# Kernel optimization log

Hardware: AMD Instinct MI355X
Metric: run time of the kernel (lower is better)

The kernel has to match this reference:

```python
import jax, jax.numpy as jnp
import numpy as np

# ---- config (mirrors AAModel init kwargs: ns=48, nv=10, sh_lmax=1) ----
N, E, NS, NV = 100000, 60000, 48, 10
SED, DED = 32, 32          # sigma / distance embedding dims
CUTOFF = 30.0              # GaussianSmearing(0, cutoff, DED)
SQ3 = float(np.sqrt(3.0))
W1_NUMEL = NS * NS + NS * NV                                   # 2784
# layer-2 fully-connected TP path weight offsets:
#   0e(x)0e->0e, 0e(x)1o->1o, 1o(x)0e->1o, 1o(x)1o->0e, 1o(x)1o->1e
O2 = [2304, 2784, 2884, 3364, 3464]


def _mlp2(x, W1, b1, W2, b2):
    return jax.nn.relu(x @ W1 + b1) @ W2 + b2


def _seg_mean(x, idx, n):
    s = jax.ops.segment_sum(x, idx, num_segments=n)
    cnt = jax.ops.segment_sum(jnp.ones(idx.shape, x.dtype), idx, num_segments=n)
    return s / jnp.maximum(cnt, 1.0).reshape((n,) + (1,) * (x.ndim - 1))


def _forward(pos, node_sigma_emb, node_s, edge_W1, edge_b1, edge_W2, edge_b2,
             fc1_W1, fc1_b1, fc1_W2, fc1_b2, fc2_W1, fc2_b1, fc2_W2, fc2_b2,
             edge_index):
    src, dst = edge_index[0], edge_index[1]
    vec = pos[dst] - pos[src]                          # [E,3]
    d = jnp.linalg.norm(vec, axis=-1)                  # [E]
    sh1 = SQ3 * vec / (d[:, None] + 1e-8)              # l=1 SH, component norm; sh0 == 1
    # Gaussian smearing of edge distances
    offsets = jnp.linspace(0.0, CUTOFF, DED)
    coeff = -0.5 / (offsets[1] - offsets[0]) ** 2
    demb = jnp.exp(coeff * (d[:, None] - offsets) ** 2)          # [E,DED]
    edge_emb = _mlp2(jnp.concatenate([node_sigma_emb[src], demb], -1),
                     edge_W1, edge_b1, edge_W2, edge_b2)         # [E,NS]

    # ---- conv layer 1:  ns x0e  (x)  1x0e+1x1o  ->  ns x0e + nv x1o ----
    xs = node_s[src]
    ea = jnp.concatenate([edge_emb, node_s[src], node_s[dst]], -1)   # [E,3*NS]
    w = _mlp2(ea, fc1_W1, fc1_b1, fc1_W2, fc1_b2)                    # [E,2784]
    w00 = w[:, :NS * NS].reshape(-1, NS, NS)
    w01 = w[:, NS * NS:].reshape(-1, NS, NV)
    inv = 1.0 / np.sqrt(NS)
    m_s = jnp.einsum('eio,ei->eo', w00, xs) * inv                    # [E,NS]
    m_v = jnp.einsum('eio,ei->eo', w01, xs)[:, :, None] * sh1[:, None, :] * inv  # [E,NV,3]
    node_s1 = node_s + _seg_mean(m_s, dst, N)                        # residual
    node_v1 = _seg_mean(m_v, dst, N)

    # ---- conv layer 2:  ns x0e + nv x1o  (x)  1x0e+1x1o  ->  ns x0e + nv x1o + nv x1e ----
    ea2 = jnp.concatenate([edge_emb, node_s1[src], node_s1[dst]], -1)
    w2 = _mlp2(ea2, fc2_W1, fc2_b1, fc2_W2, fc2_b2)                  # [E,3464]
    w00 = w2[:, :O2[0]].reshape(-1, NS, NS)
    w01 = w2[:, O2[0]:O2[1]].reshape(-1, NS, NV)
    w10 = w2[:, O2[1]:O2[2]].reshape(-1, NV, NV)
    w11s = w2[:, O2[2]:O2[3]].reshape(-1, NV, NS)
    w11p = w2[:, O2[3]:O2[4]].reshape(-1, NV, NV)
    xs, xv = node_s1[src], node_v1[src]
    nA = 1.0 / np.sqrt(2 * NS)
    nB = 1.0 / np.sqrt(2 * NV)
    m_s = (jnp.einsum('eio,ei->eo', w00, xs) * nA
           + jnp.einsum('eio,eid,ed->eo', w11s, xv, sh1) * (nB / SQ3))
    m_v = (jnp.einsum('eio,ei->eo', w01, xs)[:, :, None] * sh1[:, None, :] * nA
           + jnp.einsum('eio,eid->eod', w10, xv) * nB)
    m_p = jnp.einsum('eio,eid->eod', w11p, jnp.cross(xv, sh1[:, None, :])) * (1.0 / np.sqrt(2.0 * NV))
    node_s2 = node_s1 + _seg_mean(m_s, dst, N)
    node_v2 = node_v1 + _seg_mean(m_v, dst, N)
    node_p = _seg_mean(m_p, dst, N)
    # final node irreps ns x0e + nv x1o + nv x1e, flattened -> [N, 108]
    return jnp.concatenate([node_s2, node_v2.reshape(N, -1), node_p.reshape(N, -1)], -1)


def setup_inputs() -> dict:
    key = jax.random.key(0)
    k = jax.random.split(key, 10)
    f32 = jnp.float32
    def lin(kk, fi, fo):
        return jax.random.normal(kk, (fi, fo), f32) / np.sqrt(fi)
    return {
        'pos': 10.0 * jax.random.normal(k[0], (N, 3), f32),
        'node_sigma_emb': jax.random.normal(k[1], (N, SED), f32),
        'node_s': jax.random.normal(k[2], (N, NS), f32),
        'edge_W1': lin(k[3], SED + DED, NS), 'edge_b1': jnp.zeros((NS,), f32),
        'edge_W2': lin(k[4], NS, NS), 'edge_b2': jnp.zeros((NS,), f32),
        'fc1_W1': lin(k[5], 3 * NS, 3 * NS), 'fc1_b1': jnp.zeros((3 * NS,), f32),
        'fc1_W2': lin(k[6], 3 * NS, W1_NUMEL), 'fc1_b2': jnp.zeros((W1_NUMEL,), f32),
        'fc2_W1': lin(k[7], 3 * NS, 3 * NS), 'fc2_b1': jnp.zeros((3 * NS,), f32),
        'fc2_W2': lin(k[8], 3 * NS, O2[-1]), 'fc2_b2': jnp.zeros((O2[-1],), f32),
        'edge_index': jax.random.randint(k[9], (2, E), 0, N, jnp.int32),
    }


def reference(pos, node_sigma_emb, node_s, edge_W1, edge_b1, edge_W2, edge_b2,
              fc1_W1, fc1_b1, fc1_W2, fc1_b2, fc2_W1, fc2_b1, fc2_W2, fc2_b2,
              edge_index):
    return _forward(pos, node_sigma_emb, node_s, edge_W1, edge_b1, edge_W2, edge_b2,
                    fc1_W1, fc1_b1, fc1_W2, fc1_b2, fc2_W1, fc2_b1, fc2_W2, fc2_b2,
                    edge_index)
```

## Files before the change

### kernel.cpp

```cpp
#include <hip/hip_runtime.h>
#include <math.h>


constexpr float SQ3f = 1.7320508075688772f;
constexpr float INV1 = 0.14433756729740643f;
constexpr float NAc  = 0.10206207261596575f;
constexpr float NBc  = 0.22360679774997896f;
constexpr float NB3  = 0.12909944487358055f;
constexpr float C20  = 0.22360679774997896f;
constexpr float RATIO= 1.2649110640673518f;
constexpr float DSP  = 30.0f/31.0f;
constexpr float GCOEF= -0.5f/(DSP*DSP);

typedef __attribute__((ext_vector_type(8))) short bf16x8;
typedef __attribute__((ext_vector_type(4))) float f32x4;

__device__ __forceinline__ unsigned short f2bf(float x) {
    unsigned u = __builtin_bit_cast(unsigned, x);
    u += 0x7fffu + ((u >> 16) & 1u);
    return (unsigned short)(u >> 16);
}

__device__ __forceinline__ int colmap(int layer, int t, int lm) {
    if (layer == 0) return t*16 + lm;
    if (layer == 1) {
        if (t < 144) { const int og=t/48, i=t-og*48; return i*48 + og*16 + lm; }
        const int i = t-144; return (lm<10) ? 2304 + i*10 + lm : -1;
    }
    if (t < 144) { const int og=t/48, i=t-og*48; return i*48 + og*16 + lm; }
    if (t < 174) { const int s=t-144, og=s/10, i=s-og*10; return 2884 + i*48 + og*16 + lm; }
    if (t < 222) { const int i=t-174; return (lm<10) ? 2304 + i*10 + lm : -1; }
    if (t < 232) { const int i=t-222; return (lm<10) ? 2784 + i*10 + lm : -1; }
    { const int i=t-232; return (lm<10) ? 3364 + i*10 + lm : -1; }
}

__global__ __launch_bounds__(256)
void cvt_swz(const float* __restrict__ W, const float* __restrict__ bias,
             short* __restrict__ Wsw, int ncol, int ntile, int layer)
{
    const int gid = blockIdx.x*256 + threadIdx.x;
    const int g = gid >> 6, lane = gid & 63;
    if (g >= ntile*5) return;
    const int tile = g/5, ks = g - tile*5;
    const int c  = colmap(layer, tile, lane & 15);
    const int k0 = ks*32 + (lane >> 4)*8;
    union { uint4 u4; unsigned short h[8]; } pk;
    #pragma unroll
    for (int j=0;j<8;j++) {
        const int k = k0 + j;
        float v = 0.f;
        if (c >= 0) {
            if (k < 144)       v = W[(size_t)k*ncol + c];
            else if (k == 144) v = bias[c];
        }
        pk.h[j] = f2bf(v);
    }
    *(uint4*)&Wsw[((size_t)g*64 + lane)*8] = pk.u4;
}

__global__ __launch_bounds__(256)
void edge_kernel(const float* __restrict__ pos, const float* __restrict__ sigma,
                 const int* __restrict__ ei,
                 const float* __restrict__ W1, const float* __restrict__ b1,
                 const float* __restrict__ W2, const float* __restrict__ b2,
                 float* __restrict__ edge_emb, float* __restrict__ sh1buf,
                 int* __restrict__ deg, int E)
{
    __shared__ float inl[4][64];
    __shared__ float hidl[4][48];
    const int w    = threadIdx.x >> 6;
    const int lane = threadIdx.x & 63;
    const int e    = blockIdx.x*4 + w;
    const bool valid = (e < E);
    const int ec = valid ? e : 0;
    const int src = ei[ec], dst = ei[E+ec];
    const float vx = pos[dst*3+0]-pos[src*3+0];
    const float vy = pos[dst*3+1]-pos[src*3+1];
    const float vz = pos[dst*3+2]-pos[src*3+2];
    const float d  = sqrtf(vx*vx+vy*vy+vz*vz);
    const float si = SQ3f/(d+1e-8f);
    const float s0 = vx*si, s1 = vy*si, s2 = vz*si;
    if (lane < 32) {
        inl[w][lane] = sigma[src*32+lane];
    } else {
        const float off  = (float)(lane-32)*DSP;
        const float diff = d - off;
        inl[w][lane] = expf(GCOEF*diff*diff);
    }
    __syncthreads();
    if (lane < 48) {
        float a = b1[lane];
        #pragma unroll 8
        for (int j=0;j<64;j++) a = fmaf(inl[w][j], W1[j*48+lane], a);
        hidl[w][lane] = fmaxf(a, 0.f);
    }
    __syncthreads();
    if (valid) {
        if (lane < 48) {
            float a = b2[lane];
            #pragma unroll 8
            for (int j=0;j<48;j++) a = fmaf(hidl[w][j], W2[j*48+lane], a);
            edge_emb[e*48+lane] = a;
        }
        if (lane == 0) atomicAdd(&deg[dst], 1);
        if (lane < 3)  sh1buf[e*4+lane] = (lane==0)?s0:((lane==1)?s1:s2);
    }
}

__device__ __forceinline__ void load_bfrag(const short* __restrict__ Wsw,
                                           int tile, int lane, bf16x8 (&b)[5]) {
    #pragma unroll
    for (int ks=0; ks<5; ks++)
        b[ks] = *(const bf16x8*)&Wsw[((size_t)(tile*5+ks)*64 + lane)*8];
}

template<typename F>
__device__ __forceinline__ void region(const short* __restrict__ Wsw, int base,
                                       int count, int wv, int lane,
                                       const bf16x8 (&ag)[2][5], F&& upd)
{
    bf16x8 bc[5], bn[5];
    int i = wv;
    if (i < count) load_bfrag(Wsw, base+i, lane, bc);
    for (; i < count; i += 4) {
        if (i+4 < count) load_bfrag(Wsw, base+i+4, lane, bn);
        f32x4 a0 = {0.f,0.f,0.f,0.f}, a1 = {0.f,0.f,0.f,0.f};
        #pragma unroll
        for (int ks=0; ks<5; ks++) {
            a0 = __builtin_amdgcn_mfma_f32_16x16x32_bf16(ag[0][ks], bc[ks], a0, 0,0,0);
            a1 = __builtin_amdgcn_mfma_f32_16x16x32_bf16(ag[1][ks], bc[ks], a1, 0,0,0);
        }
        upd(i, a0, a1);
        #pragma unroll
        for (int ks=0; ks<5; ks++) bc[ks] = bn[ks];
    }
}

template<int LAYER>
__global__ __launch_bounds__(256, 2)
void conv_kernel(const float* __restrict__ edge_emb, const float* __restrict__ sh1buf,
                 const int* __restrict__ ei,
                 const float* __restrict__ sin_, const float* __restrict__ vin,
                 const short* __restrict__ W1sw, const short* __restrict__ W2sw,
                 float* __restrict__ outS, float* __restrict__ outV, int E)
{
    constexpr int POOL_FL = (LAYER==1) ? 7552 : 8960;
    __shared__ __align__(16) float pool[POOL_FL];
    __shared__ __align__(16) short hidB[32*192];
    __shared__ float xsL[32*49];
    __shared__ float sh1l[32][4];
    __shared__ int   srcl[32], dstl[32];
    __shared__ float xvL[LAYER==2 ? 32*30 : 1];
    __shared__ float uL [LAYER==2 ? 32*10 : 1];
    __shared__ float cvL[LAYER==2 ? 32*30 : 1];

    short* eaB = (short*)pool;

    const int t  = threadIdx.x;
    const int eb = blockIdx.x * 32;

    if (t < 32) {
        const int ge = eb + t; const int gc = (ge < E) ? ge : (E-1);
        srcl[t] = ei[gc]; dstl[t] = ei[E+gc];
    }
    if (t < 128) {
        const int e = t >> 2, k = t & 3;
        const int ge = eb + e; const int gc = (ge<E)?ge:(E-1);
        sh1l[e][k] = sh1buf[gc*4 + k];
    }
    __syncthreads();

    for (int p = t; p < 32*24; p += 256) {
        const int m = p / 24, s = p - m*24;
        const int k0 = s*8;
        float vals[8] = {0.f,0.f,0.f,0.f,0.f,0.f,0.f,0.f};
        if (k0 < 48) {
            const int ge = eb + m; const int gc = (ge<E)?ge:(E-1);
            const float4 a = *(const float4*)&edge_emb[gc*48 + k0];
            const float4 b = *(const float4*)&edge_emb[gc*48 + k0 + 4];
            vals[0]=a.x; vals[1]=a.y; vals[2]=a.z; vals[3]=a.w;
            vals[4]=b.x; vals[5]=b.y; vals[6]=b.z; vals[7]=b.w;
        } else if (k0 < 96) {
            const float4 a = *(const float4*)&sin_[srcl[m]*48 + (k0-48)];
            const float4 b = *(const float4*)&sin_[srcl[m]*48 + (k0-48) + 4];
            vals[0]=a.x; vals[1]=a.y; vals[2]=a.z; vals[3]=a.w;
            vals[4]=b.x; vals[5]=b.y; vals[6]=b.z; vals[7]=b.w;
            #pragma unroll
            for (int j=0;j<8;j++) xsL[m*49 + (k0-48) + j] = vals[j];
        } else if (k0 < 144) {
            const float4 a = *(const float4*)&sin_[dstl[m]*48 + (k0-96)];
            const float4 b = *(const float4*)&sin_[dstl[m]*48 + (k0-96) + 4];
            vals[0]=a.x; vals[1]=a.y; vals[2]=a.z; vals[3]=a.w;
            vals[4]=b.x; vals[5]=b.y; vals[6]=b.z; vals[7]=b.w;
        } else if (k0 == 144) {
            vals[0] = 1.f;
        }
        union { uint4 u4; unsigned short h[8]; } pk;
        #pragma unroll
        for (int j=0;j<8;j++) pk.h[j] = f2bf(vals[j]);
        *(uint4*)&eaB[m*192 + ((s ^ (m&7))*8)] = pk.u4;
    }
    if (t < 64) {
        const int m = t >> 1, s = 18 + (t & 1);
        union { uint4 u4; unsigned short h[8]; } pk;
        pk.u4.x = pk.u4.y = pk.u4.z = pk.u4.w = 0u;
        if (s == 18) pk.h[0] = f2bf(1.f);
        *(uint4*)&hidB[m*192 + ((s ^ (m&7))*8)] = pk.u4;
    }
    if (LAYER==2) {
        for (int p=t; p<320; p+=256) {
            const int e = p/10, i = p - e*10;
            const float* vp = &vin[srcl[e]*30 + i*3];
            const float x0=vp[0], x1=vp[1], x2=vp[2];
            const float h0=sh1l[e][0], h1=sh1l[e][1], h2=sh1l[e][2];
            xvL[e*30+i*3+0]=x0; xvL[e*30+i*3+1]=x1; xvL[e*30+i*3+2]=x2;
            uL[e*10+i] = x0*h0 + x1*h1 + x2*h2;
            cvL[e*30+i*3+0] = x1*h2 - x2*h1;
            cvL[e*30+i*3+1] = x2*h0 - x0*h2;
            cvL[e*30+i*3+2] = x0*h1 - x1*h0;
        }
    }
    __syncthreads();

    const int wv = t >> 6, lane = t & 63;
    const int lm = lane & 15, lk = lane >> 4;
    const int lk4 = lk*4;

    {
        bf16x8 af[2][5];
        #pragma unroll
        for (int mt=0; mt<2; mt++) {
            const int m = mt*16 + lm;
            #pragma unroll
            for (int ks=0; ks<5; ks++)
                af[mt][ks] = *(const bf16x8*)&eaB[m*192 + (((ks*4+lk) ^ (m&7))*8)];
        }
        for (int nt = wv; nt < 9; nt += 4) {
            bf16x8 bf_[5];
            load_bfrag(W1sw, nt, lane, bf_);
            f32x4 a0 = {0.f,0.f,0.f,0.f}, a1 = {0.f,0.f,0.f,0.f};
            #pragma unroll
            for (int ks=0; ks<5; ks++) {
                a0 = __builtin_amdgcn_mfma_f32_16x16x32_bf16(af[0][ks], bf_[ks], a0, 0,0,0);
                a1 = __builtin_amdgcn_mfma_f32_16x16x32_bf16(af[1][ks], bf_[ks], a1, 0,0,0);
            }
            const int c = nt*16 + lm;
            #pragma unroll
            for (int r=0; r<4; r++) {
                const int m0 = lk4 + r, m1 = 16 + lk4 + r;
                hidB[m0*192 + (((c>>3) ^ (m0&7))*8) + (c&7)] = (short)f2bf(fmaxf(a0[r], 0.f));
                hidB[m1*192 + (((c>>3) ^ (m1&7))*8) + (c&7)] = (short)f2bf(fmaxf(a1[r], 0.f));
            }
        }
    }
    __syncthreads();

    bf16x8 ag[2][5];
    #pragma unroll
    for (int mt=0; mt<2; mt++) {
        const int m = mt*16 + lm;
        #pragma unroll
        for (int ks=0; ks<5; ks++)
            ag[mt][ks] = *(const bf16x8*)&hidB[m*192 + (((ks*4+lk) ^ (m&7))*8)];
    }

    for (int og=0; og<3; og++) {
        float ms[2][4] = {{0.f,0.f,0.f,0.f},{0.f,0.f,0.f,0.f}};
        region(W2sw, og*48, 48, wv, lane, ag, [&](int i, f32x4 a0, f32x4 a1) {
            #pragma unroll
            for (int r=0; r<4; r++) {
                ms[0][r] = fmaf(a0[r], xsL[(lk4+r)*49 + i],      ms[0][r]);
                ms[1][r] = fmaf(a1[r], xsL[(16+lk4+r)*49 + i],   ms[1][r]);
            }
        });
        if (LAYER==2) {
            region(W2sw, 144+og*10, 10, wv, lane, ag, [&](int i, f32x4 a0, f32x4 a1) {
                #pragma unroll
                for (int r=0; r<4; r++) {
                    ms[0][r] = fmaf(a0[r]*RATIO, uL[(lk4+r)*10 + i],    ms[0][r]);
                    ms[1][r] = fmaf(a1[r]*RATIO, uL[(16+lk4+r)*10 + i], ms[1][r]);
                }
            });
        }
        #pragma unroll
        for (int r=0; r<4; r++) {
            pool[wv*1568 + (lk4+r)*49    + og*16+lm] = ms[0][r];
            pool[wv*1568 + (16+lk4+r)*49 + og*16+lm] = ms[1][r];
        }
    }

    if (LAYER==1) {
        float mv[2][4] = {{0.f,0.f,0.f,0.f},{0.f,0.f,0.f,0.f}};
        region(W2sw, 144, 48, wv, lane, ag, [&](int i, f32x4 a0, f32x4 a1) {
            #pragma unroll
            for (int r=0; r<4; r++) {
                mv[0][r] = fmaf(a0[r], xsL[(lk4+r)*49 + i],    mv[0][r]);
                mv[1][r] = fmaf(a1[r], xsL[(16+lk4+r)*49 + i], mv[1][r]);
            }
        });
        if (lm < 10) {
            #pragma unroll
            for (int r=0; r<4; r++) {
                pool[6272 + wv*320 + (lk4+r)*10    + lm] = mv[0][r];
                pool[6272 + wv*320 + (16+lk4+r)*10 + lm] = mv[1][r];
            }
        }
        __syncthreads();
        for (int p=t; p<1536; p+=256) {
            const int e = p/48, o = p - (p/48)*48;
            if (eb+e < E) {
                const int a = e*49 + o;
                const float v = pool[a] + pool[1568+a] + pool[3136+a] + pool[4704+a];
                unsafeAtomicAdd(&outS[dstl[e]*48 + o], v*INV1);
            }
        }
        for (int p=t; p<320; p+=256) {
            const int e = p/10, o = p - (p/10)*10;
            if (eb+e < E) {
                const int a = 6272 + e*10 + o;
                float v = pool[a] + pool[a+320] + pool[a+640] + pool[a+960];
                v *= INV1;
                #pragma unroll
                for (int d=0; d<3; d++)
                    unsafeAtomicAdd(&outV[dstl[e]*30 + o*3 + d], v*sh1l[e][d]);
            }
        }
    } else {
        __syncthreads();
        for (int p=t; p<1536; p+=256) {
            const int e = p/48, o = p - (p/48)*48;
            if (eb+e < E) {
                const int a = e*49 + o;
                const float v = pool[a] + pool[1568+a] + pool[3136+a] + pool[4704+a];
                unsafeAtomicAdd(&outS[dstl[e]*108 + o], v*NAc);
            }
        }
        __syncthreads();

        {
            float mv[2][4] = {{0.f,0.f,0.f,0.f},{0.f,0.f,0.f,0.f}};
            region(W2sw, 174, 48, wv, lane, ag, [&](int i, f32x4 a0, f32x4 a1) {
                #pragma unroll
                for (int r=0; r<4; r++) {
                    mv[0][r] = fmaf(a0[r], xsL[(lk4+r)*49 + i],    mv[0][r]);
                    mv[1][r] = fmaf(a1[r], xsL[(16+lk4+r)*49 + i], mv[1][r]);
                }
            });
            if (lm < 10) {
                #pragma unroll
                for (int r=0; r<4; r++) {
                    pool[wv*320 + (lk4+r)*10    + lm] = mv[0][r];
                    pool[wv*320 + (16+lk4+r)*10 + lm] = mv[1][r];
                }
            }
        }
        {
            float m3[2][4][3] = {};
            region(W2sw, 222, 10, wv, lane, ag, [&](int i, f32x4 a0, f32x4 a1) {
                #pragma unroll
                for (int r=0; r<4; r++)
                    #pragma unroll
                    for (int d=0; d<3; d++) {
                        m3[0][r][d] = fmaf(a0[r], xvL[(lk4+r)*30 + i*3 + d],    m3[0][r][d]);
                        m3[1][r][d] = fmaf(a1[r], xvL[(16+lk4+r)*30 + i*3 + d], m3[1][r][d]);
                    }
            });
            if (lm < 10) {
                #pragma unroll
                for (int r=0; r<4; r++)
                    #pragma unroll
                    for (int d=0; d<3; d++) {
                        pool[1280 + wv*960 + (lk4+r)*30    + lm*3 + d] = m3[0][r][d];
                        pool[1280 + wv*960 + (16+lk4+r)*30 + lm*3 + d] = m3[1][r][d];
                    }
            }
        }
        {
            float m3[2][4][3] = {};
            region(W2sw, 232, 10, wv, lane, ag, [&](int i, f32x4 a0, f32x4 a1) {
                #pragma unroll
                for (int r=0; r<4; r++)
                    #pragma unroll
                    for (int d=0; d<3; d++) {
                        m3[0][r][d] = fmaf(a0[r], cvL[(lk4+r)*30 + i*3 + d],    m3[0][r][d]);
                        m3[1][r][d] = fmaf(a1[r], cvL[(16+lk4+r)*30 + i*3 + d], m3[1][r][d]);
                    }
            });
            if (lm < 10) {
                #pragma unroll
                for (int r=0; r<4; r++)
                    #pragma unroll
                    for (int d=0; d<3; d++) {
                        pool[5120 + wv*960 + (lk4+r)*30    + lm*3 + d] = m3[0][r][d];
                        pool[5120 + wv*960 + (16+lk4+r)*30 + lm*3 + d] = m3[1][r][d];
                    }
            }
        }
        __syncthreads();
        for (int p=t; p<320; p+=256) {
            const int e = p/10, o = p - (p/10)*10;
            if (eb+e < E) {
                const int a = e*10 + o;
                const float vc = pool[a] + pool[a+320] + pool[a+640] + pool[a+960];
                const int base = dstl[e]*108;
                #pragma unroll
                for (int d=0; d<3; d++) {
                    const int b = e*30 + o*3 + d;
                    const float vv = pool[1280+b] + pool[1280+960+b] + pool[1280+1920+b] + pool[1280+2880+b];
                    const float pp = pool[5120+b] + pool[5120+960+b] + pool[5120+1920+b] + pool[5120+2880+b];
                    unsafeAtomicAdd(&outS[base + 48 + o*3 + d], vc*NAc*sh1l[e][d] + vv*NBc);
                    unsafeAtomicAdd(&outS[base + 78 + o*3 + d], pp*C20);
                }
            }
        }
    }
}

__global__ __launch_bounds__(256)
void fin1_kernel(const float* __restrict__ node_s, const int* __restrict__ deg,
                 float* __restrict__ s1, float* __restrict__ v1, int Nn)
{
    const int p = blockIdx.x*256 + threadIdx.x;
    const int totS = Nn*48;
    if (p < totS) {
        const int n = p/48;
        const int dgi = deg[n];
        const float dg = (float)(dgi > 1 ? dgi : 1);
        s1[p] = node_s[p] + s1[p]/dg;
    } else {
        const int q = p - totS;
        if (q < Nn*30) {
            const int n = q/30;
            const int dgi = deg[n];
            const float dg = (float)(dgi > 1 ? dgi : 1);
            v1[q] = v1[q]/dg;
        }
    }
}

__global__ __launch_bounds__(256)
void fin2_kernel(const float* __restrict__ s1, const float* __restrict__ v1,
                 const int* __restrict__ deg, float* __restrict__ out, int Nn)
{
    const int p = blockIdx.x*256 + threadIdx.x;
    if (p >= Nn*108) return;
    const int n = p/108, c = p - n*108;
    const int dgi = deg[n];
    const float dg = (float)(dgi > 1 ? dgi : 1);
    const float acc = out[p]/dg;
    if (c < 48)      out[p] = s1[n*48+c] + acc;
    else if (c < 78) out[p] = v1[n*30 + (c-48)] + acc;
    else             out[p] = acc;
}

extern "C" void kernel_launch(void* const* d_in, const int* in_sizes, int n_in,
                              void* d_out, int out_size, void* d_ws, size_t ws_size,
                              hipStream_t stream)
{
    const float* pos    = (const float*)d_in[0];
    const float* sigma  = (const float*)d_in[1];
    const float* node_s = (const float*)d_in[2];
    const float* eW1  = (const float*)d_in[3];
    const float* eb1  = (const float*)d_in[4];
    const float* eW2  = (const float*)d_in[5];
    const float* eb2  = (const float*)d_in[6];
    const float* f1W1 = (const float*)d_in[7];
    const float* f1b1 = (const float*)d_in[8];
    const float* f1W2 = (const float*)d_in[9];
    const float* f1b2 = (const float*)d_in[10];
    const float* f2W1 = (const float*)d_in[11];
    const float* f2b1 = (const float*)d_in[12];
    const float* f2W2 = (const float*)d_in[13];
    const float* f2b2 = (const float*)d_in[14];
    const int*   ei   = (const int*)d_in[15];
    const int Nn = in_sizes[0]/3;
    const int E  = in_sizes[15]/2;
    float* out = (float*)d_out;

    char* ws = (char*)d_ws;
    float* edge_emb = (float*)ws;  ws += (size_t)E*48*sizeof(float);
    float* sh1buf   = (float*)ws;  ws += (size_t)E*4*sizeof(float);
    float* s1       = (float*)ws;  ws += (size_t)Nn*48*sizeof(float);
    float* v1       = (float*)ws;  ws += (size_t)Nn*30*sizeof(float);
    int*   deg      = (int*)ws;    ws += (size_t)Nn*sizeof(int);
    short* W1sw     = (short*)ws;  ws += (size_t)9*5*64*8*sizeof(short);
    short* W2sw     = (short*)ws;  ws += (size_t)242*5*64*8*sizeof(short);

    hipMemsetAsync(s1,  0, (size_t)Nn*48*sizeof(float), stream);
    hipMemsetAsync(v1,  0, (size_t)Nn*30*sizeof(float), stream);
    hipMemsetAsync(deg, 0, (size_t)Nn*sizeof(int),      stream);
    hipMemsetAsync(out, 0, (size_t)Nn*108*sizeof(float), stream);

    edge_kernel<<<(E+3)/4, 256, 0, stream>>>(pos, sigma, ei, eW1, eb1, eW2, eb2,
                                             edge_emb, sh1buf, deg, E);

    cvt_swz<<<(9*5*64+255)/256,   256, 0, stream>>>(f1W1, f1b1, W1sw, 144, 9, 0);
    cvt_swz<<<(192*5*64+255)/256, 256, 0, stream>>>(f1W2, f1b2, W2sw, 2784, 192, 1);

    conv_kernel<1><<<(E+31)/32, 256, 0, stream>>>(edge_emb, sh1buf, ei, node_s, nullptr,
                                                  W1sw, W2sw, s1, v1, E);
    fin1_kernel<<<((size_t)Nn*78 + 255)/256, 256, 0, stream>>>(node_s, deg, s1, v1, Nn);

    cvt_swz<<<(9*5*64+255)/256,   256, 0, stream>>>(f2W1, f2b1, W1sw, 144, 9, 0);
    cvt_swz<<<(242*5*64+255)/256, 256, 0, stream>>>(f2W2, f2b2, W2sw, 3464, 242, 2);

    conv_kernel<2><<<(E+31)/32, 256, 0, stream>>>(edge_emb, sh1buf, ei, s1, v1,
                                                  W1sw, W2sw, out, nullptr, E);
    fin2_kernel<<<((size_t)Nn*108 + 255)/256, 256, 0, stream>>>(s1, v1, deg, out, Nn);
}
```

Baseline: 428.6 us.

## Assign output groups to waves and atomically scatter directly from MFMA registers

Instead of each of the four waves taking a strided share of every weight tile and then reducing partial sums through a large shared-memory pool, each wave now owns whole output groups. Waves 0-2 each handle one 16-column scalar slice and wave 3 handles the vector paths, and each wave issues global atomics straight from its accumulators. Per-edge scalar and vector inputs are stored transposed in LDS so they can be read as float4 vectors, and the weight fragments are double-buffered explicitly. Dropping the pool frees LDS and removes barriers, so the occupancy hint rises from 2 to 4 blocks per CU, at the cost of uneven work across waves in layer 2.

```diff
diff --git a/kernel.cpp b/kernel.cpp
--- a/kernel.cpp
+++ b/kernel.cpp
@@ -6,7 +6,6 @@
 constexpr float INV1 = 0.14433756729740643f;
 constexpr float NAc  = 0.10206207261596575f;
 constexpr float NBc  = 0.22360679774997896f;
-constexpr float NB3  = 0.12909944487358055f;
 constexpr float C20  = 0.22360679774997896f;
 constexpr float RATIO= 1.2649110640673518f;
 constexpr float DSP  = 30.0f/31.0f;
@@ -114,47 +113,33 @@
         b[ks] = *(const bf16x8*)&Wsw[((size_t)(tile*5+ks)*64 + lane)*8];
 }
 
-template<typename F>
-__device__ __forceinline__ void region(const short* __restrict__ Wsw, int base,
-                                       int count, int wv, int lane,
-                                       const bf16x8 (&ag)[2][5], F&& upd)
-{
-    bf16x8 bc[5], bn[5];
-    int i = wv;
-    if (i < count) load_bfrag(Wsw, base+i, lane, bc);
-    for (; i < count; i += 4) {
-        if (i+4 < count) load_bfrag(Wsw, base+i+4, lane, bn);
-        f32x4 a0 = {0.f,0.f,0.f,0.f}, a1 = {0.f,0.f,0.f,0.f};
-        #pragma unroll
-        for (int ks=0; ks<5; ks++) {
-            a0 = __builtin_amdgcn_mfma_f32_16x16x32_bf16(ag[0][ks], bc[ks], a0, 0,0,0);
-            a1 = __builtin_amdgcn_mfma_f32_16x16x32_bf16(ag[1][ks], bc[ks], a1, 0,0,0);
-        }
-        upd(i, a0, a1);
-        #pragma unroll
-        for (int ks=0; ks<5; ks++) bc[ks] = bn[ks];
+__device__ __forceinline__ void mfma5(const bf16x8 (&ag)[2][5], const bf16x8 (&b)[5],
+                                      f32x4& a0, f32x4& a1) {
+    a0 = (f32x4){0.f,0.f,0.f,0.f};
+    a1 = (f32x4){0.f,0.f,0.f,0.f};
+    #pragma unroll
+    for (int ks=0; ks<5; ks++) {
+        a0 = __builtin_amdgcn_mfma_f32_16x16x32_bf16(ag[0][ks], b[ks], a0, 0,0,0);
+        a1 = __builtin_amdgcn_mfma_f32_16x16x32_bf16(ag[1][ks], b[ks], a1, 0,0,0);
     }
 }
 
 template<int LAYER>
-__global__ __launch_bounds__(256, 2)
+__global__ __launch_bounds__(256, 4)
 void conv_kernel(const float* __restrict__ edge_emb, const float* __restrict__ sh1buf,
                  const int* __restrict__ ei,
                  const float* __restrict__ sin_, const float* __restrict__ vin,
                  const short* __restrict__ W1sw, const short* __restrict__ W2sw,
                  float* __restrict__ outS, float* __restrict__ outV, int E)
 {
-    constexpr int POOL_FL = (LAYER==1) ? 7552 : 8960;
-    __shared__ __align__(16) float pool[POOL_FL];
+    __shared__ __align__(16) short eaB[32*192];
     __shared__ __align__(16) short hidB[32*192];
-    __shared__ float xsL[32*49];
+    __shared__ __align__(16) float xsT[48][32];
     __shared__ float sh1l[32][4];
     __shared__ int   srcl[32], dstl[32];
-    __shared__ float xvL[LAYER==2 ? 32*30 : 1];
-    __shared__ float uL [LAYER==2 ? 32*10 : 1];
-    __shared__ float cvL[LAYER==2 ? 32*30 : 1];
-
-    short* eaB = (short*)pool;
+    __shared__ __align__(16) float xvT[LAYER==2 ? 30 : 1][32];
+    __shared__ __align__(16) float uT [LAYER==2 ? 10 : 1][32];
+    __shared__ __align__(16) float cvT[LAYER==2 ? 30 : 1][32];
 
     const int t  = threadIdx.x;
     const int eb = blockIdx.x * 32;
@@ -185,8 +170,6 @@
             const float4 b = *(const float4*)&sin_[srcl[m]*48 + (k0-48) + 4];
             vals[0]=a.x; vals[1]=a.y; vals[2]=a.z; vals[3]=a.w;
             vals[4]=b.x; vals[5]=b.y; vals[6]=b.z; vals[7]=b.w;
-            #pragma unroll
-            for (int j=0;j<8;j++) xsL[m*49 + (k0-48) + j] = vals[j];
         } else if (k0 < 144) {
             const float4 a = *(const float4*)&sin_[dstl[m]*48 + (k0-96)];
             const float4 b = *(const float4*)&sin_[dstl[m]*48 + (k0-96) + 4];
@@ -207,24 +190,28 @@
         if (s == 18) pk.h[0] = f2bf(1.f);
         *(uint4*)&hidB[m*192 + ((s ^ (m&7))*8)] = pk.u4;
     }
+    for (int p=t; p<1536; p+=256) {
+        const int k = p >> 5, e = p & 31;
+        xsT[k][e] = sin_[srcl[e]*48 + k];
+    }
     if (LAYER==2) {
         for (int p=t; p<320; p+=256) {
-            const int e = p/10, i = p - e*10;
-            const float* vp = &vin[srcl[e]*30 + i*3];
-            const float x0=vp[0], x1=vp[1], x2=vp[2];
+            const int i = p >> 5, e = p & 31;
+            const float x0 = vin[srcl[e]*30 + i*3+0];
+            const float x1 = vin[srcl[e]*30 + i*3+1];
+            const float x2 = vin[srcl[e]*30 + i*3+2];
             const float h0=sh1l[e][0], h1=sh1l[e][1], h2=sh1l[e][2];
-            xvL[e*30+i*3+0]=x0; xvL[e*30+i*3+1]=x1; xvL[e*30+i*3+2]=x2;
-            uL[e*10+i] = x0*h0 + x1*h1 + x2*h2;
-            cvL[e*30+i*3+0] = x1*h2 - x2*h1;
-            cvL[e*30+i*3+1] = x2*h0 - x0*h2;
-            cvL[e*30+i*3+2] = x0*h1 - x1*h0;
+            xvT[i*3+0][e]=x0; xvT[i*3+1][e]=x1; xvT[i*3+2][e]=x2;
+            uT[i][e] = x0*h0 + x1*h1 + x2*h2;
+            cvT[i*3+0][e] = x1*h2 - x2*h1;
+            cvT[i*3+1][e] = x2*h0 - x0*h2;
+            cvT[i*3+2][e] = x0*h1 - x1*h0;
         }
     }
     __syncthreads();
 
     const int wv = t >> 6, lane = t & 63;
-    const int lm = lane & 15, lk = lane >> 4;
-    const int lk4 = lk*4;
+    const int lm = lane & 15, lk = lane >> 4, lk4 = lk*4;
 
     {
         bf16x8 af[2][5];
@@ -236,14 +223,10 @@
                 af[mt][ks] = *(const bf16x8*)&eaB[m*192 + (((ks*4+lk) ^ (m&7))*8)];
         }
         for (int nt = wv; nt < 9; nt += 4) {
-            bf16x8 bf_[5];
-            load_bfrag(W1sw, nt, lane, bf_);
-            f32x4 a0 = {0.f,0.f,0.f,0.f}, a1 = {0.f,0.f,0.f,0.f};
-            #pragma unroll
-            for (int ks=0; ks<5; ks++) {
-                a0 = __builtin_amdgcn_mfma_f32_16x16x32_bf16(af[0][ks], bf_[ks], a0, 0,0,0);
-                a1 = __builtin_amdgcn_mfma_f32_16x16x32_bf16(af[1][ks], bf_[ks], a1, 0,0,0);
-            }
+            bf16x8 bw[5];
+            load_bfrag(W1sw, nt, lane, bw);
+            f32x4 a0, a1;
+            mfma5(af, bw, a0, a1);
             const int c = nt*16 + lm;
             #pragma unroll
             for (int r=0; r<4; r++) {
@@ -264,152 +247,219 @@
             ag[mt][ks] = *(const bf16x8*)&hidB[m*192 + (((ks*4+lk) ^ (m&7))*8)];
     }
 
-    for (int og=0; og<3; og++) {
+    if (wv < 3) {
         float ms[2][4] = {{0.f,0.f,0.f,0.f},{0.f,0.f,0.f,0.f}};
-        region(W2sw, og*48, 48, wv, lane, ag, [&](int i, f32x4 a0, f32x4 a1) {
-            #pragma unroll
-            for (int r=0; r<4; r++) {
-                ms[0][r] = fmaf(a0[r], xsL[(lk4+r)*49 + i],      ms[0][r]);
-                ms[1][r] = fmaf(a1[r], xsL[(16+lk4+r)*49 + i],   ms[1][r]);
-            }
-        });
+        {
+            bf16x8 b0[5], b1_[5];
+            const int base = wv*48;
+            load_bfrag(W2sw, base, lane, b0);
+            for (int i=0; i<48; i+=2) {
+                load_bfrag(W2sw, base+i+1, lane, b1_);
+                f32x4 a0, a1;
+                mfma5(ag, b0, a0, a1);
+                {
+                    const f32x4 x0 = *(const f32x4*)&xsT[i][lk4];
+                    const f32x4 x1 = *(const f32x4*)&xsT[i][16+lk4];
+                    #pragma unroll
+                    for (int r=0;r<4;r++) {
+                        ms[0][r] = fmaf(a0[r], x0[r], ms[0][r]);
+                        ms[1][r] = fmaf(a1[r], x1[r], ms[1][r]);
+                    }
+                }
+                if (i+2 < 48) load_bfrag(W2sw, base+i+2, lane, b0);
+                mfma5(ag, b1_, a0, a1);
+                {
+                    const f32x4 x0 = *(const f32x4*)&xsT[i+1][lk4];
+                    const f32x4 x1 = *(const f32x4*)&xsT[i+1][16+lk4];
+                    #pragma unroll
+                    for (int r=0;r<4;r++) {
+                        ms[0][r] = fmaf(a0[r], x0[r], ms[0][r]);
+                        ms[1][r] = fmaf(a1[r], x1[r], ms[1][r]);
+                    }
+                }
+            }
+        }
         if (LAYER==2) {
-            region(W2sw, 144+og*10, 10, wv, lane, ag, [&](int i, f32x4 a0, f32x4 a1) {
-                #pragma unroll
-                for (int r=0; r<4; r++) {
-                    ms[0][r] = fmaf(a0[r]*RATIO, uL[(lk4+r)*10 + i],    ms[0][r]);
-                    ms[1][r] = fmaf(a1[r]*RATIO, uL[(16+lk4+r)*10 + i], ms[1][r]);
-                }
-            });
-        }
+            bf16x8 b0[5], b1_[5];
+            const int base = 144 + wv*10;
+            load_bfrag(W2sw, base, lane, b0);
+            for (int i=0; i<10; i+=2) {
+                load_bfrag(W2sw, base+i+1, lane, b1_);
+                f32x4 a0, a1;
+                mfma5(ag, b0, a0, a1);
+                {
+                    const f32x4 u0 = *(const f32x4*)&uT[i][lk4];
+                    const f32x4 u1 = *(const f32x4*)&uT[i][16+lk4];
+                    #pragma unroll
+                    for (int r=0;r<4;r++) {
+                        ms[0][r] = fmaf(a0[r]*RATIO, u0[r], ms[0][r]);
+                        ms[1][r] = fmaf(a1[r]*RATIO, u1[r], ms[1][r]);
+                    }
+                }
+                if (i+2 < 10) load_bfrag(W2sw, base+i+2, lane, b0);
+                mfma5(ag, b1_, a0, a1);
+                {
+                    const f32x4 u0 = *(const f32x4*)&uT[i+1][lk4];
+                    const f32x4 u1 = *(const f32x4*)&uT[i+1][16+lk4];
+                    #pragma unroll
+                    for (int r=0;r<4;r++) {
+                        ms[0][r] = fmaf(a0[r]*RATIO, u0[r], ms[0][r]);
+                        ms[1][r] = fmaf(a1[r]*RATIO, u1[r], ms[1][r]);
+                    }
+                }
+            }
+        }
+        const float scale = (LAYER==1) ? INV1 : NAc;
+        const int   strd  = (LAYER==1) ? 48 : 108;
+        const int o = wv*16 + lm;
         #pragma unroll
-        for (int r=0; r<4; r++) {
-            pool[wv*1568 + (lk4+r)*49    + og*16+lm] = ms[0][r];
-            pool[wv*1568 + (16+lk4+r)*49 + og*16+lm] = ms[1][r];
-        }
-    }
-
-    if (LAYER==1) {
-        float mv[2][4] = {{0.f,0.f,0.f,0.f},{0.f,0.f,0.f,0.f}};
-        region(W2sw, 144, 48, wv, lane, ag, [&](int i, f32x4 a0, f32x4 a1) {
-            #pragma unroll
-            for (int r=0; r<4; r++) {
-                mv[0][r] = fmaf(a0[r], xsL[(lk4+r)*49 + i],    mv[0][r]);
-                mv[1][r] = fmaf(a1[r], xsL[(16+lk4+r)*49 + i], mv[1][r]);
-            }
-        });
-        if (lm < 10) {
-            #pragma unroll
-            for (int r=0; r<4; r++) {
-                pool[6272 + wv*320 + (lk4+r)*10    + lm] = mv[0][r];
-                pool[6272 + wv*320 + (16+lk4+r)*10 + lm] = mv[1][r];
-            }
-        }
-        __syncthreads();
-        for (int p=t; p<1536; p+=256) {
-            const int e = p/48, o = p - (p/48)*48;
-            if (eb+e < E) {
-                const int a = e*49 + o;
-                const float v = pool[a] + pool[1568+a] + pool[3136+a] + pool[4704+a];
-                unsafeAtomicAdd(&outS[dstl[e]*48 + o], v*INV1);
-            }
-        }
-        for (int p=t; p<320; p+=256) {
-            const int e = p/10, o = p - (p/10)*10;
-            if (eb+e < E) {
-                const int a = 6272 + e*10 + o;
-                float v = pool[a] + pool[a+320] + pool[a+640] + pool[a+960];
-                v *= INV1;
-                #pragma unroll
-                for (int d=0; d<3; d++)
-                    unsafeAtomicAdd(&outV[dstl[e]*30 + o*3 + d], v*sh1l[e][d]);
-            }
+        for (int r=0;r<4;r++) {
+            const int e0 = lk4+r, e1 = 16+lk4+r;
+            if (eb+e0 < E) unsafeAtomicAdd(&outS[(size_t)dstl[e0]*strd + o], ms[0][r]*scale);
+            if (eb+e1 < E) unsafeAtomicAdd(&outS[(size_t)dstl[e1]*strd + o], ms[1][r]*scale);
         }
     } else {
-        __syncthreads();
-        for (int p=t; p<1536; p+=256) {
-            const int e = p/48, o = p - (p/48)*48;
-            if (eb+e < E) {
-                const int a = e*49 + o;
-                const float v = pool[a] + pool[1568+a] + pool[3136+a] + pool[4704+a];
-                unsafeAtomicAdd(&outS[dstl[e]*108 + o], v*NAc);
-            }
-        }
-        __syncthreads();
-
+        float vc[2][4] = {{0.f,0.f,0.f,0.f},{0.f,0.f,0.f,0.f}};
         {
-            float mv[2][4] = {{0.f,0.f,0.f,0.f},{0.f,0.f,0.f,0.f}};
-            region(W2sw, 174, 48, wv, lane, ag, [&](int i, f32x4 a0, f32x4 a1) {
-                #pragma unroll
-                for (int r=0; r<4; r++) {
-                    mv[0][r] = fmaf(a0[r], xsL[(lk4+r)*49 + i],    mv[0][r]);
-                    mv[1][r] = fmaf(a1[r], xsL[(16+lk4+r)*49 + i], mv[1][r]);
-                }
-            });
+            bf16x8 b0[5], b1_[5];
+            const int base = (LAYER==1) ? 144 : 174;
+            load_bfrag(W2sw, base, lane, b0);
+            for (int i=0; i<48; i+=2) {
+                load_bfrag(W2sw, base+i+1, lane, b1_);
+                f32x4 a0, a1;
+                mfma5(ag, b0, a0, a1);
+                {
+                    const f32x4 x0 = *(const f32x4*)&xsT[i][lk4];
+                    const f32x4 x1 = *(const f32x4*)&xsT[i][16+lk4];
+                    #pragma unroll
+                    for (int r=0;r<4;r++) {
+                        vc[0][r] = fmaf(a0[r], x0[r], vc[0][r]);
+                        vc[1][r] = fmaf(a1[r], x1[r], vc[1][r]);
+                    }
+                }
+                if (i+2 < 48) load_bfrag(W2sw, base+i+2, lane, b0);
+                mfma5(ag, b1_, a0, a1);
+                {
+                    const f32x4 x0 = *(const f32x4*)&xsT[i+1][lk4];
+                    const f32x4 x1 = *(const f32x4*)&xsT[i+1][16+lk4];
+                    #pragma unroll
+                    for (int r=0;r<4;r++) {
+                        vc[0][r] = fmaf(a0[r], x0[r], vc[0][r]);
+                        vc[1][r] = fmaf(a1[r], x1[r], vc[1][r]);
+                    }
+                }
+            }
+        }
+        if (LAYER==1) {
             if (lm < 10) {
                 #pragma unroll
-                for (int r=0; r<4; r++) {
-                    pool[wv*320 + (lk4+r)*10    + lm] = mv[0][r];
-                    pool[wv*320 + (16+lk4+r)*10 + lm] = mv[1][r];
-                }
-            }
-        }
-        {
+                for (int r=0;r<4;r++) {
+                    const int e0 = lk4+r, e1 = 16+lk4+r;
+                    const float v0 = vc[0][r]*INV1, v1 = vc[1][r]*INV1;
+                    #pragma unroll
+                    for (int d=0; d<3; d++) {
+                        if (eb+e0 < E) unsafeAtomicAdd(&outV[(size_t)dstl[e0]*30 + lm*3 + d], v0*sh1l[e0][d]);
+                        if (eb+e1 < E) unsafeAtomicAdd(&outV[(size_t)dstl[e1]*30 + lm*3 + d], v1*sh1l[e1][d]);
+                    }
+                }
+            }
+        } else {
             float m3[2][4][3] = {};
-            region(W2sw, 222, 10, wv, lane, ag, [&](int i, f32x4 a0, f32x4 a1) {
-                #pragma unroll
-                for (int r=0; r<4; r++)
-                    #pragma unroll
-                    for (int d=0; d<3; d++) {
-                        m3[0][r][d] = fmaf(a0[r], xvL[(lk4+r)*30 + i*3 + d],    m3[0][r][d]);
-                        m3[1][r][d] = fmaf(a1[r], xvL[(16+lk4+r)*30 + i*3 + d], m3[1][r][d]);
-                    }
-            });
+            {
+                bf16x8 b0[5], b1_[5];
+                load_bfrag(W2sw, 222, lane, b0);
+                for (int i=0; i<10; i+=2) {
+                    load_bfrag(W2sw, 222+i+1, lane, b1_);
+                    f32x4 a0, a1;
+                    mfma5(ag, b0, a0, a1);
+                    #pragma unroll
+                    for (int d=0; d<3; d++) {
+                        const f32x4 x0 = *(const f32x4*)&xvT[i*3+d][lk4];
+                        const f32x4 x1 = *(const f32x4*)&xvT[i*3+d][16+lk4];
+                        #pragma unroll
+                        for (int r=0;r<4;r++) {
+                            m3[0][r][d] = fmaf(a0[r], x0[r], m3[0][r][d]);
+                            m3[1][r][d] = fmaf(a1[r], x1[r], m3[1][r][d]);
+                        }
+                    }
+                    if (i+2 < 10) load_bfrag(W2sw, 222+i+2, lane, b0);
+                    mfma5(ag, b1_, a0, a1);
+                    #pragma unroll
+                    for (int d=0; d<3; d++) {
+                        const f32x4 x0 = *(const f32x4*)&xvT[(i+1)*3+d][lk4];
+                        const f32x4 x1 = *(const f32x4*)&xvT[(i+1)*3+d][16+lk4];
+                        #pragma unroll
+                        for (int r=0;r<4;r++) {
+                            m3[0][r][d] = fmaf(a0[r], x0[r], m3[0][r][d]);
+                            m3[1][r][d] = fmaf(a1[r], x1[r], m3[1][r][d]);
+                        }
+                    }
+                }
+            }
             if (lm < 10) {
                 #pragma unroll
-                for (int r=0; r<4; r++)
-                    #pragma unroll
-                    for (int d=0; d<3; d++) {
-                        pool[1280 + wv*960 + (lk4+r)*30    + lm*3 + d] = m3[0][r][d];
-                        pool[1280 + wv*960 + (16+lk4+r)*30 + lm*3 + d] = m3[1][r][d];
-                    }
-            }
-        }
-        {
-            float m3[2][4][3] = {};
-            region(W2sw, 232, 10, wv, lane, ag, [&](int i, f32x4 a0, f32x4 a1) {
+                for (int r=0;r<4;r++) {
+                    const int e0 = lk4+r, e1 = 16+lk4+r;
+                    const float v0 = vc[0][r]*NAc, v1 = vc[1][r]*NAc;
+                    #pragma unroll
+                    for (int d=0; d<3; d++) {
+                        if (eb+e0 < E)
+                            unsafeAtomicAdd(&outS[(size_t)dstl[e0]*108 + 48 + lm*3 + d],
+                                            v0*sh1l[e0][d] + m3[0][r][d]*NBc);
+                        if (eb+e1 < E)
+                            unsafeAtomicAdd(&outS[(size_t)dstl[e1]*108 + 48 + lm*3 + d],
+                                            v1*sh1l[e1][d] + m3[1][r][d]*NBc);
+                    }
+                }
+            }
+            #pragma unroll
+            for (int a=0;a<2;a++)
                 #pragma unroll
-                for (int r=0; r<4; r++)
-                    #pragma unroll
-                    for (int d=0; d<3; d++) {
-                        m3[0][r][d] = fmaf(a0[r], cvL[(lk4+r)*30 + i*3 + d],    m3[0][r][d]);
-                        m3[1][r][d] = fmaf(a1[r], cvL[(16+lk4+r)*30 + i*3 + d], m3[1][r][d]);
-                    }
-            });
+                for (int r=0;r<4;r++)
+                    #pragma unroll
+                    for (int d=0;d<3;d++) m3[a][r][d] = 0.f;
+            {
+                bf16x8 b0[5], b1_[5];
+                load_bfrag(W2sw, 232, lane, b0);
+                for (int i=0; i<10; i+=2) {
+                    load_bfrag(W2sw, 232+i+1, lane, b1_);
+                    f32x4 a0, a1;
+                    mfma5(ag, b0, a0, a1);
+                    #pragma unroll
+                    for (int d=0; d<3; d++) {
+                        const f32x4 x0 = *(const f32x4*)&cvT[i*3+d][lk4];
+                        const f32x4 x1 = *(const f32x4*)&cvT[i*3+d][16+lk4];
+                        #pragma unroll
+                        for (int r=0;r<4;r++) {
+                            m3[0][r][d] = fmaf(a0[r], x0[r], m3[0][r][d]);
+                            m3[1][r][d] = fmaf(a1[r], x1[r], m3[1][r][d]);
+                        }
+                    }
+                    if (i+2 < 10) load_bfrag(W2sw, 232+i+2, lane, b0);
+                    mfma5(ag, b1_, a0, a1);
+                    #pragma unroll
+                    for (int d=0; d<3; d++) {
+                        const f32x4 x0 = *(const f32x4*)&cvT[(i+1)*3+d][lk4];
+                        const f32x4 x1 = *(const f32x4*)&cvT[(i+1)*3+d][16+lk4];
+                        #pragma unroll
+                        for (int r=0;r<4;r++) {
+                            m3[0][r][d] = fmaf(a0[r], x0[r], m3[0][r][d]);
+                            m3[1][r][d] = fmaf(a1[r], x1[r], m3[1][r][d]);
+                        }
+                    }
+                }
+            }
             if (lm < 10) {
                 #pragma unroll
-                for (int r=0; r<4; r++)
-                    #pragma unroll
-                    for (int d=0; d<3; d++) {
-                        pool[5120 + wv*960 + (lk4+r)*30    + lm*3 + d] = m3[0][r][d];
-                        pool[5120 + wv*960 + (16+lk4+r)*30 + lm*3 + d] = m3[1][r][d];
-                    }
-            }
-        }
-        __syncthreads();
-        for (int p=t; p<320; p+=256) {
-            const int e = p/10, o = p - (p/10)*10;
-            if (eb+e < E) {
-                const int a = e*10 + o;
-                const float vc = pool[a] + pool[a+320] + pool[a+640] + pool[a+960];
-                const int base = dstl[e]*108;
-                #pragma unroll
-                for (int d=0; d<3; d++) {
-                    const int b = e*30 + o*3 + d;
-                    const float vv = pool[1280+b] + pool[1280+960+b] + pool[1280+1920+b] + pool[1280+2880+b];
-                    const float pp = pool[5120+b] + pool[5120+960+b] + pool[5120+1920+b] + pool[5120+2880+b];
-                    unsafeAtomicAdd(&outS[base + 48 + o*3 + d], vc*NAc*sh1l[e][d] + vv*NBc);
-                    unsafeAtomicAdd(&outS[base + 78 + o*3 + d], pp*C20);
+                for (int r=0;r<4;r++) {
+                    const int e0 = lk4+r, e1 = 16+lk4+r;
+                    #pragma unroll
+                    for (int d=0; d<3; d++) {
+                        if (eb+e0 < E)
+                            unsafeAtomicAdd(&outS[(size_t)dstl[e0]*108 + 78 + lm*3 + d], m3[0][r][d]*C20);
+                        if (eb+e1 < E)
+                            unsafeAtomicAdd(&outS[(size_t)dstl[e1]*108 + 78 + lm*3 + d], m3[1][r][d]*C20);
+                    }
                 }
             }
         }
```

Measured after the change: 1.361 ms. +217.6%, slower.
